# Kernel tuning notes

Measured on AMD Instinct MI355X. Metric: run time of the kernel, lower is better.

Reference implementation:

```python
import jax, jax.numpy as jnp
import numpy as np
from jax import lax

B, S, I, H, O = 2048, 125, 2, 300, 2
NOISE_STD = 0.01


def setup_inputs() -> dict:
    key = jax.random.key(0)
    ks = jax.random.split(key, 8)
    k = 1.0 / np.sqrt(H)  # torch RNNCell / Linear uniform init bound
    return {
        "x": jax.random.normal(ks[0], (B, S, I), dtype=jnp.float32),
        "noise": jax.random.normal(ks[1], (B, S, H), dtype=jnp.float32),
        "W_ih": jax.random.uniform(ks[2], (H, I), jnp.float32, -k, k),
        "b_ih": jax.random.uniform(ks[3], (H,), jnp.float32, -k, k),
        "W_hh": jax.random.uniform(ks[4], (H, H), jnp.float32, -k, k),
        "b_hh": jax.random.uniform(ks[5], (H,), jnp.float32, -k, k),
        "W_out": jax.random.uniform(ks[6], (O, H), jnp.float32, -k, k),
        "b_out": jax.random.uniform(ks[7], (O,), jnp.float32, -k, k),
    }


def reference(x, noise, W_ih, b_ih, W_hh, b_hh, W_out, b_out):
    # x: [B,S,I], noise: [B,S,H]
    batch = x.shape[0]
    hidden = W_hh.shape[0]
    # Precompute the input-to-hidden projection for all timesteps at once.
    xin = jnp.einsum("bsi,hi->sbh", x, W_ih) + b_ih  # [S,B,H]
    noise_t = jnp.swapaxes(noise, 0, 1) * jnp.asarray(NOISE_STD, x.dtype)  # [S,B,H]

    def step(h, inp):
        xt, nt = inp
        # torch RNNCell(relu): h' = relu(x@W_ih^T + b_ih + h@W_hh^T + b_hh)
        h = jax.nn.relu(xt + h @ W_hh.T + b_hh) + nt
        return h, h

    h0 = jnp.zeros((batch, hidden), x.dtype)
    _, hs = lax.scan(step, h0, (xin, noise_t))  # hs: [S,B,H]
    # Per-step output linear, batched over all timesteps.
    out = jnp.einsum("sbh,oh->bso", hs, W_out) + b_out  # [B,S,O]
    return out
```

## Files before the change

### kernel.cpp

```cpp
#include <hip/hip_runtime.h>
#include <stdint.h>


#define SEQ   125
#define HID   300
#define APAD  328
#define KT    10
#define WAVES 10
#define NTH   (WAVES * 64)
#define RPW   8
#define NCH   600
#define NSLAB 2408

typedef __attribute__((ext_vector_type(8))) short bf16x8;
typedef __attribute__((ext_vector_type(4))) float f32x4;

__device__ __forceinline__ short f2bf(float f) {
  union { float f; uint32_t u; } v; v.f = f;
  uint32_t r = (v.u + 0x7fffu + ((v.u >> 16) & 1u)) >> 16;
  return (short)r;
}

__device__ __forceinline__ uint32_t cvt_pk_bf16(float lo, float hi) {
  uint32_t r;
  asm("v_cvt_pk_bf16_f32 %0, %1, %2" : "=v"(r) : "v"(lo), "v"(hi));
  return r;
}

__device__ __forceinline__ void dma16(const float* g, float* l) {
  __builtin_amdgcn_global_load_lds(
      (const __attribute__((address_space(1))) unsigned int*)g,
      (__attribute__((address_space(3))) unsigned int*)l, 16, 0, 0);
}

#define STEP_BARRIER() \
  asm volatile("s_waitcnt vmcnt(1) lgkmcnt(0)\n\ts_barrier" ::: "memory")

__global__ __launch_bounds__(NTH)
__attribute__((amdgpu_waves_per_eu(3, 3)))
void rnn_fused(
    const float* __restrict__ x,
    const float* __restrict__ noise,
    const float* __restrict__ W_ih,
    const float* __restrict__ b_ih,
    const float* __restrict__ W_hh,
    const float* __restrict__ b_hh,
    const float* __restrict__ W_out,
    const float* __restrict__ b_out,
    float* __restrict__ out)
{
  __shared__ __align__(16) short Abuf[2][9][APAD];
  __shared__ __align__(16) float Nbuf[3][NSLAB];
  __shared__ float xbuf[RPW][SEQ * 2];
  __shared__ float outbuf[RPW][SEQ * 2];

  const int tid  = threadIdx.x;
  const int wave = tid >> 6;
  const int lane = tid & 63;
  const int grp  = lane >> 4;
  const int lc   = lane & 15;
  const int row0 = blockIdx.x * RPW;
  const int grp8 = grp * 8;
  const int arow = (lc < 8) ? lc : 8;
  const bool lcr = (lc < 8);
  const bool w9  = (wave == 9);
  const int cb0  = wave * 32 + grp * 4;
  const int nb0  = lc * HID + cb0;

  for (int i = tid; i < 2 * 9 * APAD / 2; i += NTH)
    ((uint32_t*)Abuf)[i] = 0u;
  for (int i = tid; i < RPW * SEQ * 2; i += NTH) {
    int r = i / (SEQ * 2), j = i % (SEQ * 2);
    xbuf[r][j] = x[(row0 + r) * (SEQ * 2) + j];
  }

  const float bout0 = b_out[0], bout1 = b_out[1];

  bf16x8 wf0[KT], wf1[KT];
#pragma unroll
  for (int t = 0; t < 2; ++t) {
    int c = wave * 32 + t * 16 + lc;
#pragma unroll
    for (int kt = 0; kt < KT; ++kt) {
      bf16x8 f;
#pragma unroll
      for (int e = 0; e < 8; ++e) {
        int k = kt * 32 + grp8 + e;
        float v = 0.f;
        if (c < HID) {
          if (k < HID)            v = W_hh[c * HID + k];
          else if (k == HID)      v = W_ih[c * 2 + 0];
          else if (k == HID + 1)  v = W_ih[c * 2 + 1];
          else if (k == HID + 2)  v = b_ih[c] + b_hh[c];
        } else if (c == HID) {
          if (k < HID)            v = W_out[k];
        } else if (c == HID + 1) {
          if (k < HID)            v = W_out[HID + k];
        }
        f[e] = f2bf(v);
      }
      if (t == 0) wf0[kt] = f; else wf1[kt] = f;
    }
  }

  const bool dma = (tid < NCH);
  const float* gsrc = dma
      ? noise + (size_t)(row0 + tid / 75) * (SEQ * HID) + (tid % 75) * 4
      : noise;

  __syncthreads();

  if (tid < 8) {
    float2 xv = *(const float2*)&x[(size_t)(row0 + tid) * (SEQ * 2)];
    *(uint32_t*)&Abuf[0][tid][300] = cvt_pk_bf16(xv.x, xv.y);
    Abuf[0][tid][302] = (short)0x3F80;
    Abuf[1][tid][302] = (short)0x3F80;
  }

  if (dma) {
    dma16(gsrc, &Nbuf[0][wave * 256]);
    dma16(gsrc + HID, &Nbuf[1][wave * 256]);
  }
  const float* gsrc2 = gsrc + 2 * HID;
  STEP_BARRIER();

  const bool xw = (wave == 0) && (grp == 0) && lcr;

#define STEPM(S, CUR, RB, WB, DO_OUT, DO_EPI, DO_X, DO_ADV, DO_DMA)            \
  {                                                                            \
    if (DO_DMA) { if (dma) dma16(gsrc2, &Nbuf[WB][wave * 256]); }              \
    if (DO_ADV) gsrc2 += HID;                                                  \
                        \
    float4 nzh0 = {0.f,0.f,0.f,0.f}, nzh1 = {0.f,0.f,0.f,0.f};                 \
    float2 xvh = {0.f, 0.f};                                                   \
    if (DO_EPI) {                                                              \
      if (w9) { if (lcr && grp < 3) nzh0 = *(const float4*)&Nbuf[RB][nb0]; }   \
      else if (lcr) {                                                          \
        nzh0 = *(const float4*)&Nbuf[RB][nb0];                                 \
        nzh1 = *(const float4*)&Nbuf[RB][nb0 + 16];                            \
      }                                                                        \
    }                                                                          \
    if (DO_X) { if (xw) xvh = *(const float2*)&xbuf[lc][((S) + 1) * 2]; }      \
    const short* Ab = &Abuf[CUR][arow][grp8];                                  \
    f32x4 t0a = {0.f,0.f,0.f,0.f}, t0b = {0.f,0.f,0.f,0.f};                    \
    f32x4 t1a = {0.f,0.f,0.f,0.f}, t1b = {0.f,0.f,0.f,0.f};                    \
    _Pragma("unroll")                                                          \
    for (int kt = 0; kt < KT; kt += 2) {                                       \
      bf16x8 ha = *(const bf16x8*)(Ab + kt * 32);                              \
      bf16x8 hb = *(const bf16x8*)(Ab + kt * 32 + 32);                         \
      t0a = __builtin_amdgcn_mfma_f32_16x16x32_bf16(wf0[kt],     ha, t0a, 0,0,0); \
      t1a = __builtin_amdgcn_mfma_f32_16x16x32_bf16(wf1[kt],     ha, t1a, 0,0,0); \
      t0b = __builtin_amdgcn_mfma_f32_16x16x32_bf16(wf0[kt + 1], hb, t0b, 0,0,0); \
      t1b = __builtin_amdgcn_mfma_f32_16x16x32_bf16(wf1[kt + 1], hb, t1b, 0,0,0); \
    }                                                                          \
    f32x4 ac0 = t0a + t0b, ac1 = t1a + t1b;                                    \
    if (w9) {                                                                  \
      if (DO_OUT) { if (grp == 3 && lcr) {                                     \
        float2 o; o.x = ac0[0] + bout0; o.y = ac0[1] + bout1;                  \
        *(float2*)&outbuf[lc][((S) - 1) * 2] = o;                              \
      } }                                                                      \
      if (DO_EPI) { if (lcr && grp < 3) {                                      \
        float h0 = fmaxf(ac0[0], 0.f) + 0.01f * nzh0.x;                        \
        float h1 = fmaxf(ac0[1], 0.f) + 0.01f * nzh0.y;                        \
        float h2 = fmaxf(ac0[2], 0.f) + 0.01f * nzh0.z;                        \
        float h3 = fmaxf(ac0[3], 0.f) + 0.01f * nzh0.w;                        \
        uint2 pk; pk.x = cvt_pk_bf16(h0, h1); pk.y = cvt_pk_bf16(h2, h3);      \
        *(uint2*)&Abuf[(CUR) ^ 1][lc][cb0] = pk;                               \
      } }                                                                      \
    } else {                                                                   \
      if (DO_EPI) { if (lcr) {                                                 \
        float a0 = fmaxf(ac0[0], 0.f) + 0.01f * nzh0.x;                        \
        float a1 = fmaxf(ac0[1], 0.f) + 0.01f * nzh0.y;                        \
        float a2 = fmaxf(ac0[2], 0.f) + 0.01f * nzh0.z;                        \
        float a3 = fmaxf(ac0[3], 0.f) + 0.01f * nzh0.w;                        \
        float b0 = fmaxf(ac1[0], 0.f) + 0.01f * nzh1.x;                        \
        float b1 = fmaxf(ac1[1], 0.f) + 0.01f * nzh1.y;                        \
        float b2 = fmaxf(ac1[2], 0.f) + 0.01f * nzh1.z;                        \
        float b3 = fmaxf(ac1[3], 0.f) + 0.01f * nzh1.w;                        \
        uint2 p0; p0.x = cvt_pk_bf16(a0, a1); p0.y = cvt_pk_bf16(a2, a3);      \
        uint2 p1; p1.x = cvt_pk_bf16(b0, b1); p1.y = cvt_pk_bf16(b2, b3);      \
        *(uint2*)&Abuf[(CUR) ^ 1][lc][cb0] = p0;                               \
        *(uint2*)&Abuf[(CUR) ^ 1][lc][cb0 + 16] = p1;                          \
      } }                                                                      \
    }                                                                          \
    if (DO_X) { if (xw) {                                                      \
      *(uint32_t*)&Abuf[(CUR) ^ 1][lc][300] = cvt_pk_bf16(xvh.x, xvh.y);       \
    } }                                                                        \
    if (DO_EPI) STEP_BARRIER();                                                \
  }

  STEPM(0, 0, 0, 2, 0, 1, 1, 1, 1);
  STEPM(1, 1, 1, 0, 1, 1, 1, 1, 1);
  STEPM(2, 0, 2, 1, 1, 1, 1, 1, 1);
  STEPM(3, 1, 0, 2, 1, 1, 1, 1, 1);
  STEPM(4, 0, 1, 0, 1, 1, 1, 1, 1);
  STEPM(5, 1, 2, 1, 1, 1, 1, 1, 1);

  for (int s = 6; s < 120; s += 6) {
    STEPM(s + 0, 0, 0, 2, 1, 1, 1, 1, 1);
    STEPM(s + 1, 1, 1, 0, 1, 1, 1, 1, 1);
    STEPM(s + 2, 0, 2, 1, 1, 1, 1, 1, 1);
    STEPM(s + 3, 1, 0, 2, 1, 1, 1, 1, 1);
    STEPM(s + 4, 0, 1, 0, 1, 1, 1, 1, 1);
    STEPM(s + 5, 1, 2, 1, 1, 1, 1, 1, 1);
  }

  STEPM(120, 0, 0, 2, 1, 1, 1, 1, 1);
  STEPM(121, 1, 1, 0, 1, 1, 1, 1, 1);
  STEPM(122, 0, 2, 1, 1, 1, 1, 0, 1);
  STEPM(123, 1, 0, 2, 1, 1, 1, 0, 1);
  STEPM(124, 0, 1, 0, 1, 1, 0, 0, 1);
  STEPM(125, 1, 2, 1, 1, 0, 0, 0, 0);

#undef STEPM

  __syncthreads();

  for (int i = tid; i < RPW * SEQ * 2; i += NTH) {
    int r = i / (SEQ * 2), j = i % (SEQ * 2);
    out[(row0 + r) * (SEQ * 2) + j] = outbuf[r][j];
  }
}

extern "C" void kernel_launch(void* const* d_in, const int* in_sizes, int n_in,
                              void* d_out, int out_size, void* d_ws, size_t ws_size,
                              hipStream_t stream) {
  const float* xp     = (const float*)d_in[0];
  const float* noise  = (const float*)d_in[1];
  const float* W_ih   = (const float*)d_in[2];
  const float* b_ih   = (const float*)d_in[3];
  const float* W_hh   = (const float*)d_in[4];
  const float* b_hh   = (const float*)d_in[5];
  const float* W_out  = (const float*)d_in[6];
  const float* b_out  = (const float*)d_in[7];
  float* outp         = (float*)d_out;

  rnn_fused<<<dim3(2048 / RPW), dim3(NTH), 0, stream>>>(
      xp, noise, W_ih, b_ih, W_hh, b_hh, W_out, b_out, outp);
}
```

Baseline: 160.3 us.

## Shrink workgroup to four waves each computing five hidden tiles per step

The recurrent step is now split across 4 waves instead of 10, each wave owning 80 hidden columns (5 MFMA tiles) held in registers, and the noise DMA is redistributed so each wave loads its own two rows with three 16-byte transfers per lane. The goal is cheaper per-step barriers among fewer waves and less idle padding in the last wave. In exchange each wave runs a longer serial MFMA chain per step with more register pressure, occupancy drops to one wave per EU, and the waitcnt threshold is raised to match the extra outstanding loads.

```diff
diff --git a/kernel.cpp b/kernel.cpp
--- a/kernel.cpp
+++ b/kernel.cpp
@@ -6,11 +6,11 @@
 #define HID   300
 #define APAD  328
 #define KT    10
-#define WAVES 10
+#define NT    5
+#define WAVES 4
 #define NTH   (WAVES * 64)
 #define RPW   8
-#define NCH   600
-#define NSLAB 2408
+#define NSLAB 2400
 
 typedef __attribute__((ext_vector_type(8))) short bf16x8;
 typedef __attribute__((ext_vector_type(4))) float f32x4;
@@ -34,10 +34,10 @@
 }
 
 #define STEP_BARRIER() \
-  asm volatile("s_waitcnt vmcnt(1) lgkmcnt(0)\n\ts_barrier" ::: "memory")
+  asm volatile("s_waitcnt vmcnt(3) lgkmcnt(0)\n\ts_barrier" ::: "memory")
 
 __global__ __launch_bounds__(NTH)
-__attribute__((amdgpu_waves_per_eu(3, 3)))
+__attribute__((amdgpu_waves_per_eu(1, 1)))
 void rnn_fused(
     const float* __restrict__ x,
     const float* __restrict__ noise,
@@ -63,9 +63,6 @@
   const int grp8 = grp * 8;
   const int arow = (lc < 8) ? lc : 8;
   const bool lcr = (lc < 8);
-  const bool w9  = (wave == 9);
-  const int cb0  = wave * 32 + grp * 4;
-  const int nb0  = lc * HID + cb0;
 
   for (int i = tid; i < 2 * 9 * APAD / 2; i += NTH)
     ((uint32_t*)Abuf)[i] = 0u;
@@ -76,10 +73,10 @@
 
   const float bout0 = b_out[0], bout1 = b_out[1];
 
-  bf16x8 wf0[KT], wf1[KT];
+  bf16x8 wf[NT][KT];
 #pragma unroll
-  for (int t = 0; t < 2; ++t) {
-    int c = wave * 32 + t * 16 + lc;
+  for (int t = 0; t < NT; ++t) {
+    int c = wave * 80 + t * 16 + lc;
 #pragma unroll
     for (int kt = 0; kt < KT; ++kt) {
       bf16x8 f;
@@ -99,14 +96,17 @@
         }
         f[e] = f2bf(v);
       }
-      if (t == 0) wf0[kt] = f; else wf1[kt] = f;
+      wf[t][kt] = f;
     }
   }
 
-  const bool dma = (tid < NCH);
-  const float* gsrc = dma
-      ? noise + (size_t)(row0 + tid / 75) * (SEQ * HID) + (tid % 75) * 4
-      : noise;
+  const int r0 = lane;
+  const int r1 = 64 + lane;
+  const int r2 = (lane < 22) ? (128 + lane) : 149;
+  const float* g0 = noise + (size_t)(row0 + 2 * wave + r0 / 75) * (SEQ * HID) + (r0 % 75) * 4;
+  const float* g1 = noise + (size_t)(row0 + 2 * wave + r1 / 75) * (SEQ * HID) + (r1 % 75) * 4;
+  const float* g2 = noise + (size_t)(row0 + 2 * wave + r2 / 75) * (SEQ * HID) + (r2 % 75) * 4;
+  float* const d0 = &Nbuf[0][wave * 600];
 
   __syncthreads();
 
@@ -117,72 +117,66 @@
     Abuf[1][tid][302] = (short)0x3F80;
   }
 
-  if (dma) {
-    dma16(gsrc, &Nbuf[0][wave * 256]);
-    dma16(gsrc + HID, &Nbuf[1][wave * 256]);
-  }
-  const float* gsrc2 = gsrc + 2 * HID;
+  dma16(g0, &Nbuf[0][wave * 600]);
+  dma16(g1, &Nbuf[0][wave * 600 + 256]);
+  if (lane < 22) dma16(g2, &Nbuf[0][wave * 600 + 512]);
+  dma16(g0 + HID, &Nbuf[1][wave * 600]);
+  dma16(g1 + HID, &Nbuf[1][wave * 600 + 256]);
+  if (lane < 22) dma16(g2 + HID, &Nbuf[1][wave * 600 + 512]);
+  int gofs = 2 * HID;
   STEP_BARRIER();
 
   const bool xw = (wave == 0) && (grp == 0) && lcr;
 
 #define STEPM(S, CUR, RB, WB, DO_OUT, DO_EPI, DO_X, DO_ADV, DO_DMA)            \
   {                                                                            \
-    if (DO_DMA) { if (dma) dma16(gsrc2, &Nbuf[WB][wave * 256]); }              \
-    if (DO_ADV) gsrc2 += HID;                                                  \
-                        \
-    float4 nzh0 = {0.f,0.f,0.f,0.f}, nzh1 = {0.f,0.f,0.f,0.f};                 \
+    if (DO_DMA) {                                                              \
+      dma16(g0 + gofs, &Nbuf[WB][wave * 600]);                                 \
+      dma16(g1 + gofs, &Nbuf[WB][wave * 600 + 256]);                           \
+      if (lane < 22) dma16(g2 + gofs, &Nbuf[WB][wave * 600 + 512]);            \
+    }                                                                          \
+    if (DO_ADV) gofs += HID;                                                   \
+         \
+    float4 nzv[NT];                                                            \
     float2 xvh = {0.f, 0.f};                                                   \
-    if (DO_EPI) {                                                              \
-      if (w9) { if (lcr && grp < 3) nzh0 = *(const float4*)&Nbuf[RB][nb0]; }   \
-      else if (lcr) {                                                          \
-        nzh0 = *(const float4*)&Nbuf[RB][nb0];                                 \
-        nzh1 = *(const float4*)&Nbuf[RB][nb0 + 16];                            \
-      }                                                                        \
+    _Pragma("unroll")                                                          \
+    for (int t = 0; t < NT; ++t) {                                             \
+      nzv[t] = (float4){0.f, 0.f, 0.f, 0.f};                                   \
+      int cbt = wave * 80 + t * 16 + grp * 4;                                  \
+      if (DO_EPI && lcr && cbt < HID)                                          \
+        nzv[t] = *(const float4*)&Nbuf[RB][lc * HID + cbt];                    \
     }                                                                          \
     if (DO_X) { if (xw) xvh = *(const float2*)&xbuf[lc][((S) + 1) * 2]; }      \
+           \
     const short* Ab = &Abuf[CUR][arow][grp8];                                  \
-    f32x4 t0a = {0.f,0.f,0.f,0.f}, t0b = {0.f,0.f,0.f,0.f};                    \
-    f32x4 t1a = {0.f,0.f,0.f,0.f}, t1b = {0.f,0.f,0.f,0.f};                    \
+    f32x4 ac[NT];                                                              \
     _Pragma("unroll")                                                          \
-    for (int kt = 0; kt < KT; kt += 2) {                                       \
-      bf16x8 ha = *(const bf16x8*)(Ab + kt * 32);                              \
-      bf16x8 hb = *(const bf16x8*)(Ab + kt * 32 + 32);                         \
-      t0a = __builtin_amdgcn_mfma_f32_16x16x32_bf16(wf0[kt],     ha, t0a, 0,0,0); \
-      t1a = __builtin_amdgcn_mfma_f32_16x16x32_bf16(wf1[kt],     ha, t1a, 0,0,0); \
-      t0b = __builtin_amdgcn_mfma_f32_16x16x32_bf16(wf0[kt + 1], hb, t0b, 0,0,0); \
-      t1b = __builtin_amdgcn_mfma_f32_16x16x32_bf16(wf1[kt + 1], hb, t1b, 0,0,0); \
+    for (int t = 0; t < NT; ++t) ac[t] = (f32x4){0.f, 0.f, 0.f, 0.f};          \
+    _Pragma("unroll")                                                          \
+    for (int kt = 0; kt < KT; ++kt) {                                          \
+      bf16x8 hh = *(const bf16x8*)(Ab + kt * 32);                              \
+      _Pragma("unroll")                                                        \
+      for (int t = 0; t < NT; ++t)                                             \
+        ac[t] = __builtin_amdgcn_mfma_f32_16x16x32_bf16(wf[t][kt], hh, ac[t], 0, 0, 0); \
     }                                                                          \
-    f32x4 ac0 = t0a + t0b, ac1 = t1a + t1b;                                    \
-    if (w9) {                                                                  \
-      if (DO_OUT) { if (grp == 3 && lcr) {                                     \
-        float2 o; o.x = ac0[0] + bout0; o.y = ac0[1] + bout1;                  \
-        *(float2*)&outbuf[lc][((S) - 1) * 2] = o;                              \
-      } }                                                                      \
-      if (DO_EPI) { if (lcr && grp < 3) {                                      \
-        float h0 = fmaxf(ac0[0], 0.f) + 0.01f * nzh0.x;                        \
-        float h1 = fmaxf(ac0[1], 0.f) + 0.01f * nzh0.y;                        \
-        float h2 = fmaxf(ac0[2], 0.f) + 0.01f * nzh0.z;                        \
-        float h3 = fmaxf(ac0[3], 0.f) + 0.01f * nzh0.w;                        \
-        uint2 pk; pk.x = cvt_pk_bf16(h0, h1); pk.y = cvt_pk_bf16(h2, h3);      \
-        *(uint2*)&Abuf[(CUR) ^ 1][lc][cb0] = pk;                               \
-      } }                                                                      \
-    } else {                                                                   \
-      if (DO_EPI) { if (lcr) {                                                 \
-        float a0 = fmaxf(ac0[0], 0.f) + 0.01f * nzh0.x;                        \
-        float a1 = fmaxf(ac0[1], 0.f) + 0.01f * nzh0.y;                        \
-        float a2 = fmaxf(ac0[2], 0.f) + 0.01f * nzh0.z;                        \
-        float a3 = fmaxf(ac0[3], 0.f) + 0.01f * nzh0.w;                        \
-        float b0 = fmaxf(ac1[0], 0.f) + 0.01f * nzh1.x;                        \
-        float b1 = fmaxf(ac1[1], 0.f) + 0.01f * nzh1.y;                        \
-        float b2 = fmaxf(ac1[2], 0.f) + 0.01f * nzh1.z;                        \
-        float b3 = fmaxf(ac1[3], 0.f) + 0.01f * nzh1.w;                        \
-        uint2 p0; p0.x = cvt_pk_bf16(a0, a1); p0.y = cvt_pk_bf16(a2, a3);      \
-        uint2 p1; p1.x = cvt_pk_bf16(b0, b1); p1.y = cvt_pk_bf16(b2, b3);      \
-        *(uint2*)&Abuf[(CUR) ^ 1][lc][cb0] = p0;                               \
-        *(uint2*)&Abuf[(CUR) ^ 1][lc][cb0 + 16] = p1;                          \
-      } }                                                                      \
-    }                                                                          \
+    if (DO_OUT) { if (wave == 3 && grp == 3 && lcr) {                          \
+      float2 o; o.x = ac[3][0] + bout0; o.y = ac[3][1] + bout1;                \
+      *(float2*)&outbuf[lc][((S) - 1) * 2] = o;                                \
+    } }                                                                        \
+    if (DO_EPI) { if (lcr) {                                                   \
+      _Pragma("unroll")                                                        \
+      for (int t = 0; t < NT; ++t) {                                           \
+        int cbt = wave * 80 + t * 16 + grp * 4;                                \
+        if (cbt < HID) {                                                       \
+          float h0 = fmaxf(ac[t][0], 0.f) + 0.01f * nzv[t].x;                  \
+          float h1 = fmaxf(ac[t][1], 0.f) + 0.01f * nzv[t].y;                  \
+          float h2 = fmaxf(ac[t][2], 0.f) + 0.01f * nzv[t].z;                  \
+          float h3 = fmaxf(ac[t][3], 0.f) + 0.01f * nzv[t].w;                  \
+          uint2 pk; pk.x = cvt_pk_bf16(h0, h1); pk.y = cvt_pk_bf16(h2, h3);    \
+          *(uint2*)&Abuf[(CUR) ^ 1][lc][cbt] = pk;                             \
+        }                                                                      \
+      }                                                                        \
+    } }                                                                        \
     if (DO_X) { if (xw) {                                                      \
       *(uint32_t*)&Abuf[(CUR) ^ 1][lc][300] = cvt_pk_bf16(xvh.x, xvh.y);       \
     } }                                                                        \
```

After: 323.6 us. 102% more time.
